# Performance work log

Hardware: AMD Instinct MI355X
Metric: run time of the kernel (lower is better)

The kernel has to match this reference:

```python
import jax, jax.numpy as jnp
import numpy as np

N_NODES = 50000
N_EDGES = 1000000
IN_C, EMB_C, HID_C, EDGE_D = 64, 64, 64, 1
NEG_SLOPE = 0.2


def _seg_softmax(logits, seg, num_segments):
    m = jax.ops.segment_max(logits, seg, num_segments=num_segments)
    e = jnp.exp(logits - m[seg])
    s = jax.ops.segment_sum(e, seg, num_segments=num_segments)
    return e / s[seg]


def _supergat_mx(x, W, att_l, att_r, bias, edge_index, num_nodes):
    # x: [N, Cin], W: [Cin, Cout]; heads=1, concat=False -> output [N, Cout]
    h = x @ W
    loop = jnp.arange(num_nodes)
    src = jnp.concatenate([edge_index[0], loop])  # j (source)
    dst = jnp.concatenate([edge_index[1], loop])  # i (target, softmax group)
    x_j = h[src]  # [E+N, Cout]
    x_i = h[dst]
    logits = jnp.sum(x_i * x_j, axis=-1)  # MX gating
    alpha = jnp.sum(x_j * att_l, axis=-1) + jnp.sum(x_i * att_r, axis=-1)
    alpha = alpha * jax.nn.sigmoid(logits)
    alpha = jax.nn.leaky_relu(alpha, NEG_SLOPE)
    alpha = _seg_softmax(alpha, dst, num_nodes)
    out = jax.ops.segment_sum(x_j * alpha[:, None], dst, num_segments=num_nodes)
    return out + bias


def setup_inputs() -> dict:
    key = jax.random.key(0)
    ks = jax.random.split(key, 16)
    s = 0.05
    inp = {
        "x": jax.random.normal(ks[0], (N_NODES, IN_C), jnp.float32),
        "edge_index": jax.random.randint(ks[1], (2, N_EDGES), 0, N_NODES, jnp.int64),
        "edge_attr": jax.random.normal(ks[2], (N_EDGES, EDGE_D), jnp.float32),
        "W1": jax.random.normal(ks[3], (IN_C, EMB_C), jnp.float32) * s,
        "att_l1": jax.random.normal(ks[4], (EMB_C,), jnp.float32) * s,
        "att_r1": jax.random.normal(ks[5], (EMB_C,), jnp.float32) * s,
        "b1": jnp.zeros((EMB_C,), jnp.float32),
        "W2": jax.random.normal(ks[6], (EMB_C, HID_C), jnp.float32) * s,
        "att_l2": jax.random.normal(ks[7], (HID_C,), jnp.float32) * s,
        "att_r2": jax.random.normal(ks[8], (HID_C,), jnp.float32) * s,
        "b2": jnp.zeros((HID_C,), jnp.float32),
        "Wm1": jax.random.normal(ks[9], (2 * HID_C + EDGE_D, HID_C), jnp.float32) * s,
        "bm1": jnp.zeros((HID_C,), jnp.float32),
        "Wm2": jax.random.normal(ks[10], (HID_C, 1), jnp.float32) * s,
        "bm2": jnp.zeros((1,), jnp.float32),
    }
    return inp


def reference(x, edge_index, edge_attr, W1, att_l1, att_r1, b1,
              W2, att_l2, att_r2, b2, Wm1, bm1, Wm2, bm2):
    n = x.shape[0]
    h = jax.nn.relu(_supergat_mx(x, W1, att_l1, att_r1, b1, edge_index, n))
    h = jax.nn.relu(_supergat_mx(h, W2, att_l2, att_r2, b2, edge_index, n))
    src_h = h[edge_index[0]]
    dst_h = h[edge_index[1]]
    e = jnp.concatenate([src_h, edge_attr, dst_h], axis=-1)  # [E, 2H+edge_dim]
    e = jax.nn.relu(e @ Wm1 + bm1)
    return e @ Wm2 + bm2  # [E, 1]
```

## Files before the change

kernel.cpp:

```cpp
#include <hip/hip_runtime.h>
#include <hip/hip_bf16.h>


#define SCAN_TPB 256
#define SCAN_EPT 8
#define SCAN_CHUNK (SCAN_TPB * SCAN_EPT)
#define NXCD 8
#define SCCH 4096

__device__ __forceinline__ float wave_reduce_sum(float v) {
#pragma unroll
    for (int off = 32; off; off >>= 1) v += __shfl_xor(v, off);
    return v;
}

__device__ __forceinline__ float alpha_of(float lg, float sl, float sr) {
    float sig = 1.f / (1.f + __expf(-lg));
    float a = (sl + sr) * sig;
    return a > 0.f ? a : 0.2f * a;
}

__device__ __forceinline__ unsigned short f2bf(float f) {
    unsigned u = __float_as_uint(f);
    u += 0x7fffu + ((u >> 16) & 1u);
    return (unsigned short)(u >> 16);
}
__device__ __forceinline__ float bfLO(unsigned u) { return __uint_as_float(u << 16); }
__device__ __forceinline__ float bfHI(unsigned u) { return __uint_as_float(u & 0xffff0000u); }

__global__ __launch_bounds__(256) void gemm64_kernel(
    const float* __restrict__ X, const float* __restrict__ W,
    float* __restrict__ Y, unsigned short* __restrict__ Ybf, int nrows,
    const float* __restrict__ att_l, const float* __restrict__ att_r,
    float* __restrict__ SL, float* __restrict__ SR)
{
    __shared__ float Wl[64 * 64];
    int tid = threadIdx.x;
    const float4* W4 = (const float4*)W;
    float4* Wl4 = (float4*)Wl;
#pragma unroll
    for (int i = 0; i < 4; ++i) Wl4[i * 256 + tid] = W4[i * 256 + tid];
    __syncthreads();

    int row = blockIdx.x * 4 + (tid >> 6);
    int col = tid & 63;
    if (row >= nrows) return;
    const float* xr = X + (size_t)row * 64;
    float acc = 0.f;
#pragma unroll
    for (int k = 0; k < 64; ++k) acc += xr[k] * Wl[k * 64 + col];
    Y[(size_t)row * 64 + col] = acc;
    Ybf[(size_t)row * 64 + col] = f2bf(acc);

    if (SL != nullptr) {
        float a = wave_reduce_sum(acc * att_l[col]);
        float b = wave_reduce_sum(acc * att_r[col]);
        if (col == 0) { SL[row] = a; SR[row] = b; }
    }
}

__global__ __launch_bounds__(256) void gemm64_dual_kernel(
    const float* __restrict__ X, const float* __restrict__ WA,
    const float* __restrict__ WB,
    unsigned short* __restrict__ Pbf, unsigned short* __restrict__ Qbf,
    int nrows)
{
    __shared__ float Wa[64 * 64];
    __shared__ float Wb[64 * 64];
    int tid = threadIdx.x;
    const float4* A4 = (const float4*)WA;
    const float4* B4 = (const float4*)WB;
    float4* a4 = (float4*)Wa;
    float4* b4 = (float4*)Wb;
#pragma unroll
    for (int i = 0; i < 4; ++i) {
        a4[i * 256 + tid] = A4[i * 256 + tid];
        b4[i * 256 + tid] = B4[i * 256 + tid];
    }
    __syncthreads();

    int row = blockIdx.x * 4 + (tid >> 6);
    int col = tid & 63;
    if (row >= nrows) return;
    const float* xr = X + (size_t)row * 64;
    float accA = 0.f, accB = 0.f;
#pragma unroll
    for (int k = 0; k < 64; ++k) {
        float xv = xr[k];
        accA += xv * Wa[k * 64 + col];
        accB += xv * Wb[k * 64 + col];
    }
    Pbf[(size_t)row * 64 + col] = f2bf(accA);
    Qbf[(size_t)row * 64 + col] = f2bf(accB);
}


__global__ __launch_bounds__(256) void hist_kernel(
    const int* __restrict__ dst, int E, int N, int* __restrict__ cnt)
{
    int xcd   = blockIdx.x & (NXCD - 1);
    int chunk = blockIdx.x >> 3;
    int lo = (int)((long)N * xcd / NXCD);
    int hi = (int)((long)N * (xcd + 1) / NXCD);
    int base = chunk * SCCH;
    int end  = base + SCCH; if (end > E) end = E;
    for (int e = base + threadIdx.x; e < end; e += 256) {
        int ji = dst[e];
        if (ji >= lo && ji < hi) atomicAdd(cnt + ji, 1);
    }
}

__global__ __launch_bounds__(SCAN_TPB) void scan_local_kernel(
    const int* __restrict__ cnt, int* __restrict__ starts,
    int* __restrict__ partials, int N)
{
    __shared__ int sh[SCAN_TPB];
    int t = threadIdx.x;
    int base = blockIdx.x * SCAN_CHUNK + t * SCAN_EPT;
    int v[SCAN_EPT];
    int sum = 0;
#pragma unroll
    for (int i = 0; i < SCAN_EPT; ++i) {
        int idx = base + i;
        v[i] = (idx < N) ? cnt[idx] : 0;
        sum += v[i];
    }
    sh[t] = sum;
    __syncthreads();
#pragma unroll
    for (int off = 1; off < SCAN_TPB; off <<= 1) {
        int u = (t >= off) ? sh[t - off] : 0;
        __syncthreads();
        sh[t] += u;
        __syncthreads();
    }
    int run = sh[t] - sum;
#pragma unroll
    for (int i = 0; i < SCAN_EPT; ++i) {
        int idx = base + i;
        if (idx < N) starts[idx] = run;
        run += v[i];
    }
    if (t == SCAN_TPB - 1) partials[blockIdx.x] = sh[SCAN_TPB - 1];
}

__global__ __launch_bounds__(SCAN_TPB) void scan_partials_kernel(
    int* __restrict__ partials, int* __restrict__ starts, int nblk, int N)
{
    __shared__ int sh[SCAN_TPB];
    int t = threadIdx.x;
    int v = (t < nblk) ? partials[t] : 0;
    sh[t] = v;
    __syncthreads();
#pragma unroll
    for (int off = 1; off < SCAN_TPB; off <<= 1) {
        int u = (t >= off) ? sh[t - off] : 0;
        __syncthreads();
        sh[t] += u;
        __syncthreads();
    }
    if (t < nblk) partials[t] = sh[t] - v;
    if (t == SCAN_TPB - 1) starts[N] = sh[SCAN_TPB - 1];
}

__global__ __launch_bounds__(SCAN_TPB) void scan_add_kernel(
    int* __restrict__ starts, int* __restrict__ cursor,
    const int* __restrict__ partials, int N)
{
    int off = partials[blockIdx.x];
    int base = blockIdx.x * SCAN_CHUNK + threadIdx.x * SCAN_EPT;
#pragma unroll
    for (int i = 0; i < SCAN_EPT; ++i) {
        int idx = base + i;
        if (idx < N) {
            int s0 = starts[idx] + off;
            starts[idx] = s0;
            cursor[idx] = s0;
        }
    }
}

__global__ __launch_bounds__(256) void scatter_kernel(
    const int* __restrict__ src, const int* __restrict__ dst, int E, int N,
    int* __restrict__ cursor, int* __restrict__ csr_src)
{
    int xcd   = blockIdx.x & (NXCD - 1);
    int chunk = blockIdx.x >> 3;
    int lo = (int)((long)N * xcd / NXCD);
    int hi = (int)((long)N * (xcd + 1) / NXCD);
    int base = chunk * SCCH;
    int end  = base + SCCH; if (end > E) end = E;
    for (int e = base + threadIdx.x; e < end; e += 256) {
        int ji = dst[e];
        if (ji >= lo && ji < hi) {
            int p = atomicAdd(cursor + ji, 1);
            csr_src[p] = src[e];
        }
    }
}

__global__ __launch_bounds__(256) void node_attn_agg_kernel(
    const float* __restrict__ h, const unsigned short* __restrict__ hbf,
    const int* __restrict__ csr_src, const int* __restrict__ starts,
    const float* __restrict__ SL, const float* __restrict__ SR,
    const float* __restrict__ bias, float* __restrict__ out, int N)
{
    int node = blockIdx.x * 4 + (threadIdx.x >> 6);
    int lane = threadIdx.x & 63;
    int g    = lane >> 3;
    int sub  = lane & 7;
    if (node >= N) return;
    int s = starts[node], t = starts[node + 1];

    const float4 hiA = *(const float4*)(h + (size_t)node * 64 + sub * 8);
    const float4 hiB = *(const float4*)(h + (size_t)node * 64 + sub * 8 + 4);
    float sri = SR[node];

    float c0 = 0.f, c1 = 0.f, c2 = 0.f, c3 = 0.f;
    float c4 = 0.f, c5 = 0.f, c6 = 0.f, c7 = 0.f;
    float ssum = 0.f;

    {
        float lg = hiA.x * hiA.x + hiA.y * hiA.y + hiA.z * hiA.z + hiA.w * hiA.w
                 + hiB.x * hiB.x + hiB.y * hiB.y + hiB.z * hiB.z + hiB.w * hiB.w;
        lg += __shfl_xor(lg, 1);
        lg += __shfl_xor(lg, 2);
        lg += __shfl_xor(lg, 4);
        float a = alpha_of(lg, SL[node], sri);
        float w = __expf(a);
        if (g == 0) {
            ssum = w;
            c0 = w * hiA.x; c1 = w * hiA.y; c2 = w * hiA.z; c3 = w * hiA.w;
            c4 = w * hiB.x; c5 = w * hiB.y; c6 = w * hiB.z; c7 = w * hiB.w;
        }
    }

    for (int k = s + g; k < t; k += 8) {
        int j = csr_src[k];
        uint4 hu = *(const uint4*)(hbf + (size_t)j * 64 + sub * 8);
        float h0 = bfLO(hu.x), h1 = bfHI(hu.x), h2 = bfLO(hu.y), h3 = bfHI(hu.y);
        float h4 = bfLO(hu.z), h5 = bfHI(hu.z), h6 = bfLO(hu.w), h7 = bfHI(hu.w);
        float slj = SL[j];
        float lg = hiA.x * h0 + hiA.y * h1 + hiA.z * h2 + hiA.w * h3
                 + hiB.x * h4 + hiB.y * h5 + hiB.z * h6 + hiB.w * h7;
        lg += __shfl_xor(lg, 1);
        lg += __shfl_xor(lg, 2);
        lg += __shfl_xor(lg, 4);
        float a = alpha_of(lg, slj, sri);
        float w = __expf(a);
        ssum += w;
        c0 += w * h0; c1 += w * h1; c2 += w * h2; c3 += w * h3;
        c4 += w * h4; c5 += w * h5; c6 += w * h6; c7 += w * h7;
    }
#pragma unroll
    for (int off = 8; off < 64; off <<= 1) {
        ssum += __shfl_xor(ssum, off);
        c0 += __shfl_xor(c0, off); c1 += __shfl_xor(c1, off);
        c2 += __shfl_xor(c2, off); c3 += __shfl_xor(c3, off);
        c4 += __shfl_xor(c4, off); c5 += __shfl_xor(c5, off);
        c6 += __shfl_xor(c6, off); c7 += __shfl_xor(c7, off);
    }

    if (g == 0) {
        const float4 bA = *(const float4*)(bias + sub * 8);
        const float4 bB = *(const float4*)(bias + sub * 8 + 4);
        float inv = 1.f / ssum;
        float4 vA, vB;
        vA.x = c0 * inv + bA.x; vA.x = vA.x > 0.f ? vA.x : 0.f;
        vA.y = c1 * inv + bA.y; vA.y = vA.y > 0.f ? vA.y : 0.f;
        vA.z = c2 * inv + bA.z; vA.z = vA.z > 0.f ? vA.z : 0.f;
        vA.w = c3 * inv + bA.w; vA.w = vA.w > 0.f ? vA.w : 0.f;
        vB.x = c4 * inv + bB.x; vB.x = vB.x > 0.f ? vB.x : 0.f;
        vB.y = c5 * inv + bB.y; vB.y = vB.y > 0.f ? vB.y : 0.f;
        vB.z = c6 * inv + bB.z; vB.z = vB.z > 0.f ? vB.z : 0.f;
        vB.w = c7 * inv + bB.w; vB.w = vB.w > 0.f ? vB.w : 0.f;
        *(float4*)(out + (size_t)node * 64 + sub * 8)     = vA;
        *(float4*)(out + (size_t)node * 64 + sub * 8 + 4) = vB;
    }
}

__global__ __launch_bounds__(256) void edge_mlp_kernel(
    const unsigned short* __restrict__ Pbf, const unsigned short* __restrict__ Qbf,
    const int* __restrict__ src, const int* __restrict__ dst,
    const float* __restrict__ edge_attr,
    const float* __restrict__ arow, const float* __restrict__ bm1,
    const float* __restrict__ wm2, const float* __restrict__ bm2,
    float* __restrict__ out, int E)
{
    long gid = (long)blockIdx.x * 256 + threadIdx.x;
    int e   = (int)(gid >> 3);
    int sub = (int)(gid & 7);
    if (e >= E) return;
    int js = src[e], ji = dst[e];

    uint4 pu = *(const uint4*)(Pbf + (size_t)js * 64 + sub * 8);
    uint4 qu = *(const uint4*)(Qbf + (size_t)ji * 64 + sub * 8);
    float ea = edge_attr[e];

    const float4 saA = *(const float4*)(arow + sub * 8);
    const float4 saB = *(const float4*)(arow + sub * 8 + 4);
    const float4 swA = *(const float4*)(wm2 + sub * 8);
    const float4 swB = *(const float4*)(wm2 + sub * 8 + 4);
    const float4 bmA = *(const float4*)(bm1 + sub * 8);
    const float4 bmB = *(const float4*)(bm1 + sub * 8 + 4);

    float y, r;
    y = bfLO(pu.x) + bfLO(qu.x) + bmA.x + ea * saA.x; y = y > 0.f ? y : 0.f; r  = y * swA.x;
    y = bfHI(pu.x) + bfHI(qu.x) + bmA.y + ea * saA.y; y = y > 0.f ? y : 0.f; r += y * swA.y;
    y = bfLO(pu.y) + bfLO(qu.y) + bmA.z + ea * saA.z; y = y > 0.f ? y : 0.f; r += y * swA.z;
    y = bfHI(pu.y) + bfHI(qu.y) + bmA.w + ea * saA.w; y = y > 0.f ? y : 0.f; r += y * swA.w;
    y = bfLO(pu.z) + bfLO(qu.z) + bmB.x + ea * saB.x; y = y > 0.f ? y : 0.f; r += y * swB.x;
    y = bfHI(pu.z) + bfHI(qu.z) + bmB.y + ea * saB.y; y = y > 0.f ? y : 0.f; r += y * swB.y;
    y = bfLO(pu.w) + bfLO(qu.w) + bmB.z + ea * saB.z; y = y > 0.f ? y : 0.f; r += y * swB.z;
    y = bfHI(pu.w) + bfHI(qu.w) + bmB.w + ea * saB.w; y = y > 0.f ? y : 0.f; r += y * swB.w;
    r += __shfl_xor(r, 1);
    r += __shfl_xor(r, 2);
    r += __shfl_xor(r, 4);
    if (sub == 0) out[e] = r + bm2[0];
}

extern "C" void kernel_launch(void* const* d_in, const int* in_sizes, int n_in,
                              void* d_out, int out_size, void* d_ws, size_t ws_size,
                              hipStream_t stream)
{
    const float* x     = (const float*)d_in[0];
    const int*   ei    = (const int*)d_in[1];
    const float* eattr = (const float*)d_in[2];
    const float* W1    = (const float*)d_in[3];
    const float* attl1 = (const float*)d_in[4];
    const float* attr1 = (const float*)d_in[5];
    const float* b1    = (const float*)d_in[6];
    const float* W2    = (const float*)d_in[7];
    const float* attl2 = (const float*)d_in[8];
    const float* attr2 = (const float*)d_in[9];
    const float* b2    = (const float*)d_in[10];
    const float* Wm1   = (const float*)d_in[11];
    const float* bm1   = (const float*)d_in[12];
    const float* Wm2   = (const float*)d_in[13];
    const float* bm2   = (const float*)d_in[14];

    int N  = in_sizes[0] / 64;
    int E  = in_sizes[1] / 2;
    const int* srcI = ei;
    const int* dstI = ei + E;

    float* ws       = (float*)d_ws;
    float* hpre     = ws;
    float* h1       = hpre + (size_t)N * 64;
    float* h2       = h1   + (size_t)N * 64;
    float* SL       = h2   + (size_t)N * 64;
    float* SR       = SL + N;
    int*   csr_src  = (int*)(SR + N);
    int*   cnt      = csr_src + E;
    int*   starts   = cnt + N;
    int*   cursor   = starts + N + 1;
    int*   partials = cursor + N;
    unsigned short* hbf = (unsigned short*)(partials + SCAN_TPB);
    unsigned short* Pbf = (unsigned short*)hpre;
    unsigned short* Qbf = (unsigned short*)h1;

    dim3 blk(256);
    int gg = (N + 3) / 4;
    int gx = NXCD * ((E + SCCH - 1) / SCCH);
    int gs = (N + SCAN_CHUNK - 1) / SCAN_CHUNK;
    int gm = (int)(((long)E * 8 + 255) / 256);

    hipMemsetAsync(cnt, 0, (size_t)N * sizeof(int), stream);
    hipLaunchKernelGGL(hist_kernel, dim3(gx), blk, 0, stream, dstI, E, N, cnt);
    hipLaunchKernelGGL(scan_local_kernel, dim3(gs), dim3(SCAN_TPB), 0, stream,
                       cnt, starts, partials, N);
    hipLaunchKernelGGL(scan_partials_kernel, dim3(1), dim3(SCAN_TPB), 0, stream,
                       partials, starts, gs, N);
    hipLaunchKernelGGL(scan_add_kernel, dim3(gs), dim3(SCAN_TPB), 0, stream,
                       starts, cursor, partials, N);
    hipLaunchKernelGGL(scatter_kernel, dim3(gx), blk, 0, stream,
                       srcI, dstI, E, N, cursor, csr_src);

    hipLaunchKernelGGL(gemm64_kernel, dim3(gg), blk, 0, stream,
                       x, W1, hpre, hbf, N, attl1, attr1, SL, SR);
    hipLaunchKernelGGL(node_attn_agg_kernel, dim3(gg), blk, 0, stream,
                       hpre, hbf, csr_src, starts, SL, SR, b1, h1, N);

    hipLaunchKernelGGL(gemm64_kernel, dim3(gg), blk, 0, stream,
                       h1, W2, hpre, hbf, N, attl2, attr2, SL, SR);
    hipLaunchKernelGGL(node_attn_agg_kernel, dim3(gg), blk, 0, stream,
                       hpre, hbf, csr_src, starts, SL, SR, b2, h2, N);

    hipLaunchKernelGGL(gemm64_dual_kernel, dim3(gg), blk, 0, stream,
                       h2, Wm1, Wm1 + 65 * 64, Pbf, Qbf, N);
    hipLaunchKernelGGL(edge_mlp_kernel, dim3(gm), blk, 0, stream,
                       Pbf, Qbf, srcI, dstI, eattr,
                       Wm1 + 64 * 64, bm1, Wm2, bm2, (float*)d_out, E);
}
```

Before: 422.0 us.

## Tile node GEMMs to 16 rows per block with float4 column outputs

The three small 64x64 node GEMM kernels now handle 16 rows per block instead of 4. Each thread computes four output columns using float4 weight reads from shared memory, and the input rows are staged in padded shared memory. This spreads the cost of loading the weight matrix across more rows, cuts repeated global reads of X, and vectorises the stores. The attention score reduction now runs over 16 lanes instead of a full wave. There are fewer blocks and more registers per thread, but these GEMMs are only a small part of the total pipeline.

```diff
diff --git a/kernel.cpp b/kernel.cpp
--- a/kernel.cpp
+++ b/kernel.cpp
@@ -7,12 +7,7 @@
 #define SCAN_CHUNK (SCAN_TPB * SCAN_EPT)
 #define NXCD 8
 #define SCCH 4096
-
-__device__ __forceinline__ float wave_reduce_sum(float v) {
-#pragma unroll
-    for (int off = 32; off; off >>= 1) v += __shfl_xor(v, off);
-    return v;
-}
+#define GR 16
 
 __device__ __forceinline__ float alpha_of(float lg, float sl, float sr) {
     float sig = 1.f / (1.f + __expf(-lg));
@@ -35,27 +30,53 @@
     float* __restrict__ SL, float* __restrict__ SR)
 {
     __shared__ float Wl[64 * 64];
+    __shared__ float Xs[GR][68];
     int tid = threadIdx.x;
-    const float4* W4 = (const float4*)W;
-    float4* Wl4 = (float4*)Wl;
-#pragma unroll
-    for (int i = 0; i < 4; ++i) Wl4[i * 256 + tid] = W4[i * 256 + tid];
+    int base = blockIdx.x * GR;
+
+    {
+        const float4* W4 = (const float4*)W;
+        float4* Wl4 = (float4*)Wl;
+#pragma unroll
+        for (int i = 0; i < 4; ++i) Wl4[i * 256 + tid] = W4[i * 256 + tid];
+        int r = tid >> 4, q = tid & 15;
+        if (base + r < nrows) {
+            float4 xv = ((const float4*)X)[(size_t)(base + r) * 16 + q];
+            Xs[r][q * 4 + 0] = xv.x; Xs[r][q * 4 + 1] = xv.y;
+            Xs[r][q * 4 + 2] = xv.z; Xs[r][q * 4 + 3] = xv.w;
+        }
+    }
     __syncthreads();
 
-    int row = blockIdx.x * 4 + (tid >> 6);
-    int col = tid & 63;
+    int r  = tid >> 4;
+    int cq = tid & 15;
+    int row = base + r;
     if (row >= nrows) return;
-    const float* xr = X + (size_t)row * 64;
-    float acc = 0.f;
-#pragma unroll
-    for (int k = 0; k < 64; ++k) acc += xr[k] * Wl[k * 64 + col];
-    Y[(size_t)row * 64 + col] = acc;
-    Ybf[(size_t)row * 64 + col] = f2bf(acc);
+
+    const float4* Wl4 = (const float4*)Wl;
+    float4 acc = make_float4(0.f, 0.f, 0.f, 0.f);
+#pragma unroll
+    for (int k = 0; k < 64; ++k) {
+        float xv = Xs[r][k];
+        float4 w4 = Wl4[k * 16 + cq];
+        acc.x += xv * w4.x; acc.y += xv * w4.y;
+        acc.z += xv * w4.z; acc.w += xv * w4.w;
+    }
+    ((float4*)Y)[(size_t)row * 16 + cq] = acc;
+    ushort4 bf;
+    bf.x = f2bf(acc.x); bf.y = f2bf(acc.y); bf.z = f2bf(acc.z); bf.w = f2bf(acc.w);
+    *(ushort4*)(Ybf + (size_t)row * 64 + cq * 4) = bf;
 
     if (SL != nullptr) {
-        float a = wave_reduce_sum(acc * att_l[col]);
-        float b = wave_reduce_sum(acc * att_r[col]);
-        if (col == 0) { SL[row] = a; SR[row] = b; }
+        const float4 al = *(const float4*)(att_l + cq * 4);
+        const float4 ar = *(const float4*)(att_r + cq * 4);
+        float a = acc.x * al.x + acc.y * al.y + acc.z * al.z + acc.w * al.w;
+        float b = acc.x * ar.x + acc.y * ar.y + acc.z * ar.z + acc.w * ar.w;
+        a += __shfl_xor(a, 1); b += __shfl_xor(b, 1);
+        a += __shfl_xor(a, 2); b += __shfl_xor(b, 2);
+        a += __shfl_xor(a, 4); b += __shfl_xor(b, 4);
+        a += __shfl_xor(a, 8); b += __shfl_xor(b, 8);
+        if (cq == 0) { SL[row] = a; SR[row] = b; }
     }
 }
 
@@ -67,31 +88,53 @@
 {
     __shared__ float Wa[64 * 64];
     __shared__ float Wb[64 * 64];
+    __shared__ float Xs[GR][68];
     int tid = threadIdx.x;
-    const float4* A4 = (const float4*)WA;
-    const float4* B4 = (const float4*)WB;
-    float4* a4 = (float4*)Wa;
-    float4* b4 = (float4*)Wb;
-#pragma unroll
-    for (int i = 0; i < 4; ++i) {
-        a4[i * 256 + tid] = A4[i * 256 + tid];
-        b4[i * 256 + tid] = B4[i * 256 + tid];
+    int base = blockIdx.x * GR;
+
+    {
+        const float4* A4 = (const float4*)WA;
+        const float4* B4 = (const float4*)WB;
+        float4* a4 = (float4*)Wa;
+        float4* b4 = (float4*)Wb;
+#pragma unroll
+        for (int i = 0; i < 4; ++i) {
+            a4[i * 256 + tid] = A4[i * 256 + tid];
+            b4[i * 256 + tid] = B4[i * 256 + tid];
+        }
+        int r = tid >> 4, q = tid & 15;
+        if (base + r < nrows) {
+            float4 xv = ((const float4*)X)[(size_t)(base + r) * 16 + q];
+            Xs[r][q * 4 + 0] = xv.x; Xs[r][q * 4 + 1] = xv.y;
+            Xs[r][q * 4 + 2] = xv.z; Xs[r][q * 4 + 3] = xv.w;
+        }
     }
     __syncthreads();
 
-    int row = blockIdx.x * 4 + (tid >> 6);
-    int col = tid & 63;
+    int r  = tid >> 4;
+    int cq = tid & 15;
+    int row = base + r;
     if (row >= nrows) return;
-    const float* xr = X + (size_t)row * 64;
-    float accA = 0.f, accB = 0.f;
+
+    const float4* Wa4 = (const float4*)Wa;
+    const float4* Wb4 = (const float4*)Wb;
+    float4 accA = make_float4(0.f, 0.f, 0.f, 0.f);
+    float4 accB = make_float4(0.f, 0.f, 0.f, 0.f);
 #pragma unroll
     for (int k = 0; k < 64; ++k) {
-        float xv = xr[k];
-        accA += xv * Wa[k * 64 + col];
-        accB += xv * Wb[k * 64 + col];
-    }
-    Pbf[(size_t)row * 64 + col] = f2bf(accA);
-    Qbf[(size_t)row * 64 + col] = f2bf(accB);
+        float xv = Xs[r][k];
+        float4 wa = Wa4[k * 16 + cq];
+        float4 wb = Wb4[k * 16 + cq];
+        accA.x += xv * wa.x; accA.y += xv * wa.y;
+        accA.z += xv * wa.z; accA.w += xv * wa.w;
+        accB.x += xv * wb.x; accB.y += xv * wb.y;
+        accB.z += xv * wb.z; accB.w += xv * wb.w;
+    }
+    ushort4 pa, qb;
+    pa.x = f2bf(accA.x); pa.y = f2bf(accA.y); pa.z = f2bf(accA.z); pa.w = f2bf(accA.w);
+    qb.x = f2bf(accB.x); qb.y = f2bf(accB.y); qb.z = f2bf(accB.z); qb.w = f2bf(accB.w);
+    *(ushort4*)(Pbf + (size_t)row * 64 + cq * 4) = pa;
+    *(ushort4*)(Qbf + (size_t)row * 64 + cq * 4) = qb;
 }
 
 
@@ -360,10 +403,11 @@
     unsigned short* Qbf = (unsigned short*)h1;
 
     dim3 blk(256);
-    int gg = (N + 3) / 4;
-    int gx = NXCD * ((E + SCCH - 1) / SCCH);
-    int gs = (N + SCAN_CHUNK - 1) / SCAN_CHUNK;
-    int gm = (int)(((long)E * 8 + 255) / 256);
+    int gg  = (N + 3) / 4;
+    int ggm = (N + GR - 1) / GR;
+    int gx  = NXCD * ((E + SCCH - 1) / SCCH);
+    int gs  = (N + SCAN_CHUNK - 1) / SCAN_CHUNK;
+    int gm  = (int)(((long)E * 8 + 255) / 256);
 
     hipMemsetAsync(cnt, 0, (size_t)N * sizeof(int), stream);
     hipLaunchKernelGGL(hist_kernel, dim3(gx), blk, 0, stream, dstI, E, N, cnt);
@@ -376,17 +420,17 @@
     hipLaunchKernelGGL(scatter_kernel, dim3(gx), blk, 0, stream,
                        srcI, dstI, E, N, cursor, csr_src);
 
-    hipLaunchKernelGGL(gemm64_kernel, dim3(gg), blk, 0, stream,
+    hipLaunchKernelGGL(gemm64_kernel, dim3(ggm), blk, 0, stream,
                        x, W1, hpre, hbf, N, attl1, attr1, SL, SR);
     hipLaunchKernelGGL(node_attn_agg_kernel, dim3(gg), blk, 0, stream,
                        hpre, hbf, csr_src, starts, SL, SR, b1, h1, N);
 
-    hipLaunchKernelGGL(gemm64_kernel, dim3(gg), blk, 0, stream,
+    hipLaunchKernelGGL(gemm64_kernel, dim3(ggm), blk, 0, stream,
                        h1, W2, hpre, hbf, N, attl2, attr2, SL, SR);
     hipLaunchKernelGGL(node_attn_agg_kernel, dim3(gg), blk, 0, stream,
                        hpre, hbf, csr_src, starts, SL, SR, b2, h2, N);
 
-    hipLaunchKernelGGL(gemm64_dual_kernel, dim3(gg), blk, 0, stream,
+    hipLaunchKernelGGL(gemm64_dual_kernel, dim3(ggm), blk, 0, stream,
                        h2, Wm1, Wm1 + 65 * 64, Pbf, Qbf, N);
     hipLaunchKernelGGL(edge_mlp_kernel, dim3(gm), blk, 0, stream,
                        Pbf, Qbf, srcI, dstI, eattr,
```

Measured after the change: 356.0 us. 1.19x faster.
